# Kernel optimization log

Measured on AMD Instinct MI355X. Metric: run time of the kernel, lower is better.

## Reference

```python
import jax, jax.numpy as jnp
import numpy as np

SCORE_THRESH = 0.5
NMS_THRESH = 0.4
TOP_K = 1000  # fixed pre-NMS candidate budget (jit-safe replacement for boolean masking)
STRIDES = (8, 16, 32)
H, W = 2176, 3840


def _anchor_centers(fh, fw, stride):
    yv, xv = jnp.meshgrid(jnp.arange(fh), jnp.arange(fw), indexing='ij')
    return (jnp.stack([xv, yv], -1).reshape(-1, 2).astype(jnp.float32)) * stride  # [N,2]


def _decode_level(scores, bbox, kps, stride):
    fh, fw = H // stride, W // stride
    c = _anchor_centers(fh, fw, stride)                 # [N,2]
    s = jax.nn.sigmoid(scores.reshape(-1))              # [N]
    d = bbox.reshape(-1, 4) * stride                    # [N,4]
    boxes = jnp.concatenate([c - d[:, :2], c + d[:, 2:4]], axis=1)  # x1y1x2y2
    k = kps.reshape(-1, 5, 2) * stride + c[:, None, :]  # (x,y) pairs
    return s, boxes, k.reshape(-1, 10)


def _iou_matrix(b):
    area = (b[:, 2] - b[:, 0]) * (b[:, 3] - b[:, 1])
    lt = jnp.maximum(b[:, None, :2], b[None, :, :2])
    rb = jnp.minimum(b[:, None, 2:], b[None, :, 2:])
    wh = jnp.clip(rb - lt, 0.0)
    inter = wh[..., 0] * wh[..., 1]
    return inter / jnp.clip(area[:, None] + area[None, :] - inter, 1e-9)


def _nms_keep(iou, valid):
    n = iou.shape[0]
    ar = jnp.arange(n)

    def body(i, keep):
        sup = (iou[i] > NMS_THRESH) & (ar > i) & keep[i]
        return keep & ~sup

    return jax.lax.fori_loop(0, n, body, valid)


def reference(x, scores8, bbox8, kps8, scores16, bbox16, kps16, scores32, bbox32, kps32):
    levels = ((scores8, bbox8, kps8), (scores16, bbox16, kps16), (scores32, bbox32, kps32))
    ss, bs, ks = [], [], []
    for (s, b, k), stride in zip(levels, STRIDES):
        si, bi, ki = _decode_level(s, b, k, stride)
        ss.append(si); bs.append(bi); ks.append(ki)
    scores = jnp.concatenate(ss)   # [N_total]
    boxes = jnp.concatenate(bs)    # [N_total,4]
    kpss = jnp.concatenate(ks)     # [N_total,10]

    masked = jnp.where(scores > SCORE_THRESH, scores, -1.0)
    top_s, idx = jax.lax.top_k(masked, TOP_K)
    valid = top_s > SCORE_THRESH
    b = boxes[idx]
    k = kpss[idx]

    keep = jax.lax.stop_gradient(_nms_keep(_iou_matrix(b), valid))
    final_boxes = jnp.where(keep[:, None], b, 0.0)
    final_scores = jnp.where(keep, top_s, 0.0)
    final_kpss = jnp.where(keep[:, None], k, 0.0)
    return final_boxes, final_scores, final_kpss


def setup_inputs() -> dict:
    key = jax.random.key(0)
    ks = jax.random.split(key, 10)
    n8 = (H // 8) * (W // 8)
    n16 = (H // 16) * (W // 16)
    n32 = (H // 32) * (W // 32)
    return {
        'x': jax.random.normal(ks[0], (1, 3, H, W), jnp.float32),
        'scores8': jax.random.normal(ks[1], (1, n8, 1), jnp.float32),
        'bbox8': jax.random.uniform(ks[2], (1, n8, 4), jnp.float32),
        'kps8': jax.random.normal(ks[3], (1, n8, 10), jnp.float32),
        'scores16': jax.random.normal(ks[4], (1, n16, 1), jnp.float32),
        'bbox16': jax.random.uniform(ks[5], (1, n16, 4), jnp.float32),
        'kps16': jax.random.normal(ks[6], (1, n16, 10), jnp.float32),
        'scores32': jax.random.normal(ks[7], (1, n32, 1), jnp.float32),
        'bbox32': jax.random.uniform(ks[8], (1, n32, 4), jnp.float32),
        'kps32': jax.random.normal(ks[9], (1, n32, 10), jnp.float32),
    }
```

## Files before the change

kernel.cpp:

```cpp
#include <hip/hip_runtime.h>
#include <stdint.h>

typedef unsigned int u32;
typedef unsigned long long u64;

#define N8   130560
#define N16  32640
#define N32  8160
#define NTOT 171360
#define NTOT4 42840
#define TOPK 1000
#define NWORDS 16
#define NBINS 4096
#define BUCKET_SCALE 682.0f
#define LIST_CAP 2048
#define NBLK 168
#define NRED 32
#define RANK_BLKS 32
#define IOU_TASKS (TOPK * NWORDS)
#define IOU_BLKS 63
#define NMS_CACHE 256
#define POISON 0xAAAAAAAAu
#define SPIN_CAP (1u << 22)


#define MI_ARRA 0
#define MI_REDA 128
#define MI_ARRB 256
#define MI_REDD 384
#define MI_B    512
#define MI_CNT  640
#define MI_CMP  768
#define MI_CMPD 896
#define MI_DEC  1024
#define MI_DECD 1152
#define MI_IOU  1280
#define META_U32 1536

#define OFF_PART 0
#define OFF_RED  1376256
#define OFF_META 1392640
#define OFF_NZ   1398784
#define OFF_LIST 1398912
#define OFF_MASK 1415296

__device__ __forceinline__ u32 ald32(const u32* p) {
  return __hip_atomic_load(p, __ATOMIC_RELAXED, __HIP_MEMORY_SCOPE_AGENT);
}
__device__ __forceinline__ u64 ald64(const u64* p) {
  return __hip_atomic_load(p, __ATOMIC_RELAXED, __HIP_MEMORY_SCOPE_AGENT);
}
__device__ __forceinline__ void ast32(u32* p, u32 v) {
  __hip_atomic_store(p, v, __ATOMIC_RELAXED, __HIP_MEMORY_SCOPE_AGENT);
}
__device__ __forceinline__ void ast64(u64* p, u64 v) {
  __hip_atomic_store(p, v, __ATOMIC_RELAXED, __HIP_MEMORY_SCOPE_AGENT);
}
__device__ __forceinline__ void publish(u32* p, u32 v) {
  __hip_atomic_store(p, v, __ATOMIC_RELEASE, __HIP_MEMORY_SCOPE_AGENT);
}
template <int SLP>
__device__ __forceinline__ u32 spin_tag(const u32* p) {
  u32 v, it = 0;
  while (((v = ald32(p)) >> 16) != 0xC0DEu) {
    __builtin_amdgcn_s_sleep(SLP);
    if (++it > SPIN_CAP) break;
  }
  return v;
}
__device__ __forceinline__ u32 normc(u32 v) {
  return v >= 0x80000000u ? v - POISON : v;
}
__device__ __forceinline__ bool arrive_last(u32* p, u32 total) {
  u32 old = __hip_atomic_fetch_add(p, 1u, __ATOMIC_RELAXED, __HIP_MEMORY_SCOPE_AGENT);
  if (normc(old) == total - 1u) { ast32(p, 0u); return true; }
  return false;
}

__device__ __forceinline__ u32 bucket_of(float x) {
  u32 b = (u32)(x * BUCKET_SCALE);
  return b > (NBINS - 1) ? (NBINS - 1) : b;
}

__device__ __forceinline__ float4 load_logit4(int v, const float* s8, const float* s16,
                                              const float* s32) {
  int e = v * 4;
  if (e < N8) return ((const float4*)s8)[v];
  if (e < N8 + N16) return ((const float4*)s16)[v - N8 / 4];
  return ((const float4*)s32)[v - (N8 + N16) / 4];
}

__device__ __forceinline__ bool iou_gt04(float4 a, float4 b) {
#pragma clang fp contract(off)
  float areaA = (a.z - a.x) * (a.w - a.y);
  float areaB = (b.z - b.x) * (b.w - b.y);
  float ltx = fmaxf(a.x, b.x);
  float lty = fmaxf(a.y, b.y);
  float rbx = fminf(a.z, b.z);
  float rby = fminf(a.w, b.w);
  float wx = rbx - ltx; wx = wx > 0.0f ? wx : 0.0f;
  float wy = rby - lty; wy = wy > 0.0f ? wy : 0.0f;
  float inter = wx * wy;
  float un = areaA + areaB - inter;
  un = un > 1e-9f ? un : 1e-9f;
  return (inter / un) > 0.4f;
}

__device__ __forceinline__ u64 valid_word(int w, u32 vcnt) {
  int lo = w * 64;
  if ((int)vcnt >= lo + 64) return ~0ull;
  if ((int)vcnt <= lo) return 0ull;
  return (1ull << (vcnt - (u32)lo)) - 1ull;
}

__global__ void __launch_bounds__(256) k_zero(u32* __restrict__ meta) {
  for (int k = threadIdx.x; k < META_U32; k += 256) meta[k] = 0;
}

__global__ void __launch_bounds__(256) k_fused(
    const float* __restrict__ s8, const float* __restrict__ s16, const float* __restrict__ s32,
    const float* __restrict__ bb8,  const float* __restrict__ kp8,
    const float* __restrict__ bb16, const float* __restrict__ kp16,
    const float* __restrict__ bb32, const float* __restrict__ kp32,
    u32* __restrict__ part, u32* red, u32* meta, u64* nzWords, u64* list, u64* mask,
    float* out) {
  __shared__ __align__(16) char smem[36864];
  __shared__ u32 sB, sCntE, sCntF, sBase;
  __shared__ u32 cnt16[16], sPc[16], sOff17[17];
  __shared__ u64 sRem[NWORDS];
  __shared__ int isLast;
  const int t = threadIdx.x, blk = blockIdx.x;
  const int wave = t >> 6, lane = t & 63;
  const int v = blk * 256 + t;
  u64* o64 = (u64*)out;

  u32* lh = (u32*)smem;
#pragma unroll
  for (int k = 0; k < 16; ++k) lh[k * 256 + t] = 0;
  __syncthreads();
  float4 x = make_float4(-1.f, -1.f, -1.f, -1.f);
  if (v < NTOT4) {
    x = load_logit4(v, s8, s16, s32);
    if (x.x > 0.0f) atomicAdd(&lh[bucket_of(x.x)], 1u);
    if (x.y > 0.0f) atomicAdd(&lh[bucket_of(x.y)], 1u);
    if (x.z > 0.0f) atomicAdd(&lh[bucket_of(x.z)], 1u);
    if (x.w > 0.0f) atomicAdd(&lh[bucket_of(x.w)], 1u);
  }
  __syncthreads();
#pragma unroll
  for (int k = 0; k < 8; ++k) {
    int w = k * 256 + t;
    ast32(&part[blk * 2048 + w], lh[2 * w] | (lh[2 * w + 1] << 16));
  }
  __syncthreads();
  if (t == 0 && arrive_last(&meta[MI_ARRA], NBLK))
    publish(&meta[MI_REDA], 0xC0DE0000u);

  if (blk < NRED) {
    u32* llo = (u32*)smem;
    u32* lhi = llo + 256;
    if (t == 0) spin_tag<2>(&meta[MI_REDA]);
    __syncthreads();
    int w = t & 63, pp = t >> 6;
    u32 lo = 0, hi = 0;
    for (int p = pp; p < NBLK; p += 4) {
      u32 pv = ald32(&part[p * 2048 + blk * 64 + w]);
      lo += pv & 0xFFFFu; hi += pv >> 16;
    }
    llo[t] = lo; lhi[t] = hi;
    __syncthreads();
    if (t < 64) {
      u32 l = llo[t] + llo[64 + t] + llo[128 + t] + llo[192 + t];
      u32 h = lhi[t] + lhi[64 + t] + lhi[128 + t] + lhi[192 + t];
      ast32(&red[blk * 128 + 2 * t], l);
      ast32(&red[blk * 128 + 2 * t + 1], h);
    }
    __syncthreads();
    if (t == 0 && arrive_last(&meta[MI_ARRB], NRED)) {
      ast32(&meta[MI_REDA], 0u);
      publish(&meta[MI_REDD], 0xC0DE0000u);
    }
  }

  if (blk == 0) {
    if (t == 0) { spin_tag<2>(&meta[MI_REDD]); ast32(&meta[MI_REDD], 0u); }
    __syncthreads();
    u32* hloc = (u32*)smem;
    u32* csum = (u32*)(smem + 16384);
#pragma unroll
    for (int k = 0; k < 16; ++k) hloc[k * 256 + t] = ald32(&red[k * 256 + t]);
    if (t < NWORDS) ast64(&nzWords[t], 0ull);
    __syncthreads();
    u32 sum = 0;
    int base = t * 16;
#pragma unroll
    for (int k = 0; k < 16; ++k) sum += hloc[base + k];
    csum[t] = sum;
    __syncthreads();
    for (int off = 1; off < 256; off <<= 1) {
      u32 add = (t + off < 256) ? csum[t + off] : 0u;
      __syncthreads();
      csum[t] += add;
      __syncthreads();
    }
    u32 above = (t < 255) ? csum[t + 1] : 0u;
    if (t == 0 && csum[0] < TOPK) ast32(&meta[MI_B], 0xC0DE0000u);
    if (csum[t] >= TOPK && above < TOPK) {
      u32 cum = above, Bv = (u32)(t * 16);
      for (int b = t * 16 + 15; b >= t * 16; --b) {
        cum += hloc[b];
        if (cum >= TOPK) { Bv = (u32)b; break; }
      }
      ast32(&meta[MI_B], 0xC0DE0000u | Bv);
    }
  }

  if (t == 0) sB = spin_tag<4>(&meta[MI_B]) & 0xFFFFu;
  __syncthreads();
  const u32 B = sB;
  u32 win = 0;
  float c[4] = {x.x, x.y, x.z, x.w};
  if (v < NTOT4) {
#pragma unroll
    for (int j = 0; j < 4; ++j)
      if (c[j] > 0.0f && bucket_of(c[j]) >= B) win |= 1u << j;
  }
  u32 wpos[4], wcnt[4];
#pragma unroll
  for (int j = 0; j < 4; ++j) {
    u64 bal = __ballot((win >> j) & 1u);
    wcnt[j] = (u32)__popcll(bal);
    wpos[j] = (u32)__popcll(bal & ((1ull << lane) - 1ull));
  }
  if (lane == 0) {
#pragma unroll
    for (int j = 0; j < 4; ++j) cnt16[wave * 4 + j] = wcnt[j];
  }
  __syncthreads();
  if (t == 0) {
    u32 tot = 0, pre[16];
#pragma unroll
    for (int k = 0; k < 16; ++k) { pre[k] = tot; tot += cnt16[k]; }
#pragma unroll
    for (int k = 0; k < 16; ++k) cnt16[k] = pre[k];
    sBase = tot ? normc(__hip_atomic_fetch_add(&meta[MI_CNT], tot, __ATOMIC_RELAXED,
                                               __HIP_MEMORY_SCOPE_AGENT))
                : 0u;
  }
  __syncthreads();
#pragma unroll
  for (int j = 0; j < 4; ++j) {
    if ((win >> j) & 1u) {
      u32 dst = sBase + cnt16[wave * 4 + j] + wpos[j];
      if (dst < LIST_CAP) {
        u32 idx = (u32)(v * 4 + j);
        ast64(&list[dst], ((u64)__float_as_uint(c[j]) << 32) | (u64)(~idx));
      }
    }
  }
  __syncthreads();
  if (t == 0 && arrive_last(&meta[MI_CMP], NBLK)) {
    u32 cc = normc(ald32(&meta[MI_CNT]));
    if (cc > LIST_CAP) cc = LIST_CAP;
    ast32(&meta[MI_CNT], 0u);
    ast32(&meta[MI_B], 0u);
    publish(&meta[MI_CMPD], 0xC0DE0000u | cc);
  }
  if (blk >= IOU_BLKS) return;

  if (blk < RANK_BLKS) {
    if (t == 0) sCntE = spin_tag<4>(&meta[MI_CMPD]) & 0xFFFFu;
    __syncthreads();
    const u32 cnt = sCntE;
    u64* keys = (u64*)smem;
    for (int j = t; j < LIST_CAP; j += 256) keys[j] = (j < (int)cnt) ? ald64(&list[j]) : 0ull;
    __syncthreads();
    if (t < 64) {
      int tid = blk * 64 + t;
      if (tid < (int)cnt) {
        u64 my = keys[tid];
        int rank = 0, j = 0;
        for (; j + 4 <= (int)cnt; j += 4)
          rank += (keys[j] > my) + (keys[j + 1] > my) + (keys[j + 2] > my) + (keys[j + 3] > my);
        for (; j < (int)cnt; ++j) rank += (keys[j] > my);
        if (rank < TOPK) {
          float lx = __uint_as_float((u32)(my >> 32));
          float sc = (float)(1.0 / (1.0 + exp(-(double)lx)));
          u32 idx = ~((u32)my);
          float4 box;
          float kv[10];
          int p, xq, yq;
          float st;
          const float *bb, *kp;
          if (idx < N8) {
            st = 8.f;  p = (int)idx;              xq = p % 480; yq = p / 480; bb = bb8;  kp = kp8;
          } else if (idx < N8 + N16) {
            st = 16.f; p = (int)idx - N8;         xq = p % 240; yq = p / 240; bb = bb16; kp = kp16;
          } else {
            st = 32.f; p = (int)idx - (N8 + N16); xq = p % 120; yq = p / 120; bb = bb32; kp = kp32;
          }
          float cx = (float)xq * st, cy = (float)yq * st;
          {
#pragma clang fp contract(off)
            float d0 = bb[4 * p + 0] * st;
            float d1 = bb[4 * p + 1] * st;
            float d2 = bb[4 * p + 2] * st;
            float d3 = bb[4 * p + 3] * st;
            box.x = cx - d0; box.y = cy - d1; box.z = cx + d2; box.w = cy + d3;
            for (int q = 0; q < 10; ++q)
              kv[q] = kp[10 * p + q] * st + ((q & 1) ? cy : cx);
          }
          ast64(&o64[2 * rank],     ((u64)__float_as_uint(box.y) << 32) | __float_as_uint(box.x));
          ast64(&o64[2 * rank + 1], ((u64)__float_as_uint(box.w) << 32) | __float_as_uint(box.z));
          ast32(&((u32*)out)[4000 + rank], __float_as_uint(sc));
          int wb = 2500 + 5 * rank;
#pragma unroll
          for (int q = 0; q < 5; ++q)
            ast64(&o64[wb + q],
                  ((u64)__float_as_uint(kv[2 * q + 1]) << 32) | __float_as_uint(kv[2 * q]));
        }
      } else if (tid < TOPK) {
        ast64(&o64[2 * tid], 0ull); ast64(&o64[2 * tid + 1], 0ull);
        ast32(&((u32*)out)[4000 + tid], 0u);
        int wb = 2500 + 5 * tid;
#pragma unroll
        for (int q = 0; q < 5; ++q) ast64(&o64[wb + q], 0ull);
      }
    }
    __syncthreads();
    if (t == 0 && arrive_last(&meta[MI_DEC], RANK_BLKS)) {
      ast32(&meta[MI_CMPD], 0u);
      publish(&meta[MI_DECD], 0xC0DE0000u | cnt);
    }
  }

  if (t == 0) sCntF = spin_tag<4>(&meta[MI_DECD]) & 0xFFFFu;
  __syncthreads();
  {
    float4* boxes = (float4*)smem;
    for (int r = t; r < TOPK; r += 256) {
      u64 a = ald64(&o64[2 * r]), b = ald64(&o64[2 * r + 1]);
      float4 bx;
      bx.x = __uint_as_float((u32)a); bx.y = __uint_as_float((u32)(a >> 32));
      bx.z = __uint_as_float((u32)b); bx.w = __uint_as_float((u32)(b >> 32));
      boxes[r] = bx;
    }
    __syncthreads();
    int task = blk * 256 + t;
    if (task < IOU_TASKS) {
      int w = task / 1000;
      int i = task - w * 1000;
      float4 a = boxes[i];
      int bse = w * 64;
      int jend = (bse + 64) < TOPK ? (bse + 64) : TOPK;
      u64 bits = 0;
      for (int j = bse; j < jend; ++j)
        if (j > i && iou_gt04(a, boxes[j])) bits |= 1ull << (j - bse);
      ast64(&mask[(u64)w * 1000 + i], bits);
      if (bits) atomicOr(&nzWords[i >> 6], 1ull << (i & 63));
    }
    __syncthreads();
    if (t == 0) {
      bool lastF = arrive_last(&meta[MI_IOU], IOU_BLKS);
      if (lastF) ast32(&meta[MI_DECD], 0u);
      isLast = lastF ? 1 : 0;
    }
    __syncthreads();
    if (!isLast) return;

    const u32 vcnt = sCntF < TOPK ? sCntF : TOPK;
    u32* rows = (u32*)smem;
    u64* cache = (u64*)(smem + 4096);
    u64 nzv = 0;
    if (t < NWORDS) {
      nzv = ald64(&nzWords[t]) & valid_word(t, vcnt);
      sPc[t] = (u32)__popcll(nzv);
    }
    __syncthreads();
    if (t == 0) {
      u32 o = 0;
      for (int w = 0; w < NWORDS; ++w) { sOff17[w] = o; o += sPc[w]; }
      sOff17[16] = o;
    }
    __syncthreads();
    if (t < NWORDS) {
      u64 m = nzv;
      u32 o = sOff17[t];
      while (m) { int b = __builtin_ctzll(m); m &= m - 1; rows[o++] = (u32)(t * 64 + b); }
    }
    __syncthreads();
    const int S = (int)sOff17[16];
    const int Sc = S < NMS_CACHE ? S : NMS_CACHE;
    for (int idx = t; idx < Sc * NWORDS; idx += 256) {
      int s = idx >> 4, w = idx & 15;
      cache[s * NWORDS + w] = ald64(&mask[(u64)w * 1000 + rows[s]]);
    }
    __syncthreads();
    if (t < 64) {
      u64 remv = 0;
      for (int s = 0; s < S; ++s) {
        u32 row = rows[s];
        int cc = (int)(row >> 6), b = (int)(row & 63);
        u64 remc = __shfl(remv, cc);
        if (!((remc >> b) & 1ull)) {
          u64 m = 0;
          if (t < NWORDS)
            m = (s < NMS_CACHE) ? cache[s * NWORDS + t] : ald64(&mask[(u64)t * 1000 + row]);
          remv |= m;
        }
      }
      if (t < NWORDS) sRem[t] = valid_word(t, vcnt) & remv;
    }
    __syncthreads();
    for (int r = t; r < TOPK; r += 256) {
      if ((sRem[r >> 6] >> (r & 63)) & 1ull) {
        ast64(&o64[2 * r], 0ull); ast64(&o64[2 * r + 1], 0ull);
        ast32(&((u32*)out)[4000 + r], 0u);
        int wb = 2500 + 5 * r;
#pragma unroll
        for (int q = 0; q < 5; ++q) ast64(&o64[wb + q], 0ull);
      }
    }
  }
}

extern "C" void kernel_launch(void* const* d_in, const int* in_sizes, int n_in,
                              void* d_out, int out_size, void* d_ws, size_t ws_size,
                              hipStream_t stream) {
  const float* s8   = (const float*)d_in[1];
  const float* bb8  = (const float*)d_in[2];
  const float* kp8  = (const float*)d_in[3];
  const float* s16  = (const float*)d_in[4];
  const float* bb16 = (const float*)d_in[5];
  const float* kp16 = (const float*)d_in[6];
  const float* s32  = (const float*)d_in[7];
  const float* bb32 = (const float*)d_in[8];
  const float* kp32 = (const float*)d_in[9];

  char* ws = (char*)d_ws;
  u32* part    = (u32*)(ws + OFF_PART);
  u32* red     = (u32*)(ws + OFF_RED);
  u32* meta    = (u32*)(ws + OFF_META);
  u64* nzWords = (u64*)(ws + OFF_NZ);
  u64* list    = (u64*)(ws + OFF_LIST);
  u64* mask    = (u64*)(ws + OFF_MASK);
  float* out   = (float*)d_out;

  k_zero<<<1, 256, 0, stream>>>(meta);
  k_fused<<<NBLK, 256, 0, stream>>>(s8, s16, s32, bb8, kp8, bb16, kp16, bb32, kp32,
                                    part, red, meta, nzWords, list, mask, out);
}
```

Baseline: 198.8 us.

## Collapse pipeline into single 63-block kernel with global-atomic histogram and split rank

Drops the separate meta-zeroing kernel and the two-level partial histogram reduction. Each of 63 blocks now loads 12 logits per thread and adds directly into a global histogram with atomics; the last-arriving block computes the threshold bucket and re-zeroes the histogram and meta for the next call. The rank stage is spread across all blocks by splitting each candidate's comparison count over 8 slices, and the publish flags are replicated 8 ways to spread spinning across cache lines. This removes one launch and several grid barriers, at the cost of contended global atomics and relying on self-reset state being correct across calls.

```diff
diff --git a/kernel.cpp b/kernel.cpp
--- a/kernel.cpp
+++ b/kernel.cpp
@@ -13,36 +13,32 @@
 #define NWORDS 16
 #define NBINS 4096
 #define BUCKET_SCALE 682.0f
-#define LIST_CAP 2048
-#define NBLK 168
-#define NRED 32
-#define RANK_BLKS 32
+#define NBLK 63
+#define NTHR 256
+#define STRIDE (NBLK*NTHR)
+#define LIST_CAP 2016
+#define CPB 32
 #define IOU_TASKS (TOPK * NWORDS)
-#define IOU_BLKS 63
 #define NMS_CACHE 256
 #define POISON 0xAAAAAAAAu
-#define SPIN_CAP (1u << 22)
+#define SPIN_CAP (1u << 20)
 
 
 #define MI_ARRA 0
-#define MI_REDA 128
-#define MI_ARRB 256
-#define MI_REDD 384
-#define MI_B    512
-#define MI_CNT  640
-#define MI_CMP  768
-#define MI_CMPD 896
-#define MI_DEC  1024
-#define MI_DECD 1152
-#define MI_IOU  1280
-#define META_U32 1536
-
-#define OFF_PART 0
-#define OFF_RED  1376256
-#define OFF_META 1392640
-#define OFF_NZ   1398784
-#define OFF_LIST 1398912
-#define OFF_MASK 1415296
+#define MI_B(c)    (128*(1+(c)))
+#define MI_CNT     (128*9)
+#define MI_CMP     (128*10)
+#define MI_CMPD(c) (128*(11+(c)))
+#define MI_DEC     (128*19)
+#define MI_DECD(c) (128*(20+(c)))
+#define MI_IOU     (128*28)
+#define META_U32   (128*29)
+
+#define OFF_HIST 0
+#define OFF_META 16384
+#define OFF_NZ   32768
+#define OFF_LIST 33024
+#define OFF_MASK 49152
 
 __device__ __forceinline__ u32 ald32(const u32* p) {
   return __hip_atomic_load(p, __ATOMIC_RELAXED, __HIP_MEMORY_SCOPE_AGENT);
@@ -113,82 +109,41 @@
   return (1ull << (vcnt - (u32)lo)) - 1ull;
 }
 
-__global__ void __launch_bounds__(256) k_zero(u32* __restrict__ meta) {
-  for (int k = threadIdx.x; k < META_U32; k += 256) meta[k] = 0;
-}
-
-__global__ void __launch_bounds__(256) k_fused(
+__global__ void __launch_bounds__(256) k_all(
     const float* __restrict__ s8, const float* __restrict__ s16, const float* __restrict__ s32,
     const float* __restrict__ bb8,  const float* __restrict__ kp8,
     const float* __restrict__ bb16, const float* __restrict__ kp16,
     const float* __restrict__ bb32, const float* __restrict__ kp32,
-    u32* __restrict__ part, u32* red, u32* meta, u64* nzWords, u64* list, u64* mask,
-    float* out) {
+    u32* hist, u32* meta, u64* nzWords, u64* list, u64* mask, float* out) {
   __shared__ __align__(16) char smem[36864];
-  __shared__ u32 sB, sCntE, sCntF, sBase;
-  __shared__ u32 cnt16[16], sPc[16], sOff17[17];
+  __shared__ u32 sB, sBpub, sCntE, sCntF, sBase;
+  __shared__ int sFind, isLast;
+  __shared__ u32 cnt48[48];
+  __shared__ u32 sPc[16], sOff17[17];
   __shared__ u64 sRem[NWORDS];
-  __shared__ int isLast;
   const int t = threadIdx.x, blk = blockIdx.x;
   const int wave = t >> 6, lane = t & 63;
-  const int v = blk * 256 + t;
   u64* o64 = (u64*)out;
 
-  u32* lh = (u32*)smem;
-#pragma unroll
-  for (int k = 0; k < 16; ++k) lh[k * 256 + t] = 0;
-  __syncthreads();
-  float4 x = make_float4(-1.f, -1.f, -1.f, -1.f);
-  if (v < NTOT4) {
-    x = load_logit4(v, s8, s16, s32);
-    if (x.x > 0.0f) atomicAdd(&lh[bucket_of(x.x)], 1u);
-    if (x.y > 0.0f) atomicAdd(&lh[bucket_of(x.y)], 1u);
-    if (x.z > 0.0f) atomicAdd(&lh[bucket_of(x.z)], 1u);
-    if (x.w > 0.0f) atomicAdd(&lh[bucket_of(x.w)], 1u);
-  }
-  __syncthreads();
-#pragma unroll
-  for (int k = 0; k < 8; ++k) {
-    int w = k * 256 + t;
-    ast32(&part[blk * 2048 + w], lh[2 * w] | (lh[2 * w + 1] << 16));
-  }
-  __syncthreads();
-  if (t == 0 && arrive_last(&meta[MI_ARRA], NBLK))
-    publish(&meta[MI_REDA], 0xC0DE0000u);
-
-  if (blk < NRED) {
-    u32* llo = (u32*)smem;
-    u32* lhi = llo + 256;
-    if (t == 0) spin_tag<2>(&meta[MI_REDA]);
-    __syncthreads();
-    int w = t & 63, pp = t >> 6;
-    u32 lo = 0, hi = 0;
-    for (int p = pp; p < NBLK; p += 4) {
-      u32 pv = ald32(&part[p * 2048 + blk * 64 + w]);
-      lo += pv & 0xFFFFu; hi += pv >> 16;
-    }
-    llo[t] = lo; lhi[t] = hi;
-    __syncthreads();
-    if (t < 64) {
-      u32 l = llo[t] + llo[64 + t] + llo[128 + t] + llo[192 + t];
-      u32 h = lhi[t] + lhi[64 + t] + lhi[128 + t] + lhi[192 + t];
-      ast32(&red[blk * 128 + 2 * t], l);
-      ast32(&red[blk * 128 + 2 * t + 1], h);
-    }
-    __syncthreads();
-    if (t == 0 && arrive_last(&meta[MI_ARRB], NRED)) {
-      ast32(&meta[MI_REDA], 0u);
-      publish(&meta[MI_REDD], 0xC0DE0000u);
-    }
-  }
-
-  if (blk == 0) {
-    if (t == 0) { spin_tag<2>(&meta[MI_REDD]); ast32(&meta[MI_REDD], 0u); }
-    __syncthreads();
+  const int v0 = blk * NTHR + t;
+  float4 x0 = load_logit4(v0, s8, s16, s32);
+  float4 x1 = load_logit4(v0 + STRIDE, s8, s16, s32);
+  float4 x2 = make_float4(-1.f, -1.f, -1.f, -1.f);
+  if (v0 + 2 * STRIDE < NTOT4) x2 = load_logit4(v0 + 2 * STRIDE, s8, s16, s32);
+  float cv[12] = {x0.x, x0.y, x0.z, x0.w, x1.x, x1.y, x1.z, x1.w,
+                  x2.x, x2.y, x2.z, x2.w};
+#pragma unroll
+  for (int j = 0; j < 12; ++j)
+    if (cv[j] > 0.0f) atomicAdd(&hist[bucket_of(cv[j])], 1u);
+  __syncthreads();
+  if (t == 0) sFind = arrive_last(&meta[MI_ARRA], NBLK) ? 1 : 0;
+  __syncthreads();
+
+  if (sFind) {
     u32* hloc = (u32*)smem;
     u32* csum = (u32*)(smem + 16384);
 #pragma unroll
-    for (int k = 0; k < 16; ++k) hloc[k * 256 + t] = ald32(&red[k * 256 + t]);
+    for (int k = 0; k < 16; ++k) hloc[k * 256 + t] = normc(ald32(&hist[k * 256 + t]));
     if (t < NWORDS) ast64(&nzWords[t], 0ull);
     __syncthreads();
     u32 sum = 0;
@@ -204,57 +159,52 @@
       __syncthreads();
     }
     u32 above = (t < 255) ? csum[t + 1] : 0u;
-    if (t == 0 && csum[0] < TOPK) ast32(&meta[MI_B], 0xC0DE0000u);
+    if (t == 0 && csum[0] < TOPK) sBpub = 0u;
     if (csum[t] >= TOPK && above < TOPK) {
       u32 cum = above, Bv = (u32)(t * 16);
       for (int b = t * 16 + 15; b >= t * 16; --b) {
         cum += hloc[b];
         if (cum >= TOPK) { Bv = (u32)b; break; }
       }
-      ast32(&meta[MI_B], 0xC0DE0000u | Bv);
-    }
-  }
-
-  if (t == 0) sB = spin_tag<4>(&meta[MI_B]) & 0xFFFFu;
+      sBpub = Bv;
+    }
+    __syncthreads();
+    if (t < 8) publish(&meta[MI_B(t)], 0xC0DE0000u | sBpub);
+#pragma unroll
+    for (int k = 0; k < 16; ++k) hist[k * 256 + t] = 0u;
+  }
+
+  if (t == 0) sB = spin_tag<8>(&meta[MI_B(blk & 7)]) & 0xFFFFu;
   __syncthreads();
   const u32 B = sB;
-  u32 win = 0;
-  float c[4] = {x.x, x.y, x.z, x.w};
-  if (v < NTOT4) {
-#pragma unroll
-    for (int j = 0; j < 4; ++j)
-      if (c[j] > 0.0f && bucket_of(c[j]) >= B) win |= 1u << j;
-  }
-  u32 wpos[4], wcnt[4];
-#pragma unroll
-  for (int j = 0; j < 4; ++j) {
-    u64 bal = __ballot((win >> j) & 1u);
-    wcnt[j] = (u32)__popcll(bal);
+  u32 winm = 0;
+#pragma unroll
+  for (int j = 0; j < 12; ++j)
+    if (cv[j] > 0.0f && bucket_of(cv[j]) >= B) winm |= 1u << j;
+  u32 wpos[12];
+#pragma unroll
+  for (int j = 0; j < 12; ++j) {
+    u64 bal = __ballot((winm >> j) & 1u);
+    if (lane == 0) cnt48[wave * 12 + j] = (u32)__popcll(bal);
     wpos[j] = (u32)__popcll(bal & ((1ull << lane) - 1ull));
   }
-  if (lane == 0) {
-#pragma unroll
-    for (int j = 0; j < 4; ++j) cnt16[wave * 4 + j] = wcnt[j];
-  }
   __syncthreads();
   if (t == 0) {
-    u32 tot = 0, pre[16];
-#pragma unroll
-    for (int k = 0; k < 16; ++k) { pre[k] = tot; tot += cnt16[k]; }
-#pragma unroll
-    for (int k = 0; k < 16; ++k) cnt16[k] = pre[k];
+    u32 tot = 0, pre;
+#pragma unroll
+    for (int k = 0; k < 48; ++k) { pre = tot; tot += cnt48[k]; cnt48[k] = pre; }
     sBase = tot ? normc(__hip_atomic_fetch_add(&meta[MI_CNT], tot, __ATOMIC_RELAXED,
                                                __HIP_MEMORY_SCOPE_AGENT))
                 : 0u;
   }
   __syncthreads();
 #pragma unroll
-  for (int j = 0; j < 4; ++j) {
-    if ((win >> j) & 1u) {
-      u32 dst = sBase + cnt16[wave * 4 + j] + wpos[j];
+  for (int j = 0; j < 12; ++j) {
+    if ((winm >> j) & 1u) {
+      u32 dst = sBase + cnt48[wave * 12 + j] + wpos[j];
       if (dst < LIST_CAP) {
-        u32 idx = (u32)(v * 4 + j);
-        ast64(&list[dst], ((u64)__float_as_uint(c[j]) << 32) | (u64)(~idx));
+        u32 idx = (u32)((v0 + (j >> 2) * STRIDE) * 4 + (j & 3));
+        ast64(&list[dst], ((u64)__float_as_uint(cv[j]) << 32) | (u64)(~idx));
       }
     }
   }
@@ -263,27 +213,43 @@
     u32 cc = normc(ald32(&meta[MI_CNT]));
     if (cc > LIST_CAP) cc = LIST_CAP;
     ast32(&meta[MI_CNT], 0u);
-    ast32(&meta[MI_B], 0u);
-    publish(&meta[MI_CMPD], 0xC0DE0000u | cc);
-  }
-  if (blk >= IOU_BLKS) return;
-
-  if (blk < RANK_BLKS) {
-    if (t == 0) sCntE = spin_tag<4>(&meta[MI_CMPD]) & 0xFFFFu;
-    __syncthreads();
-    const u32 cnt = sCntE;
+#pragma unroll
+    for (int c = 0; c < 8; ++c) ast32(&meta[MI_B(c)], 0u);
+#pragma unroll
+    for (int c = 0; c < 8; ++c) publish(&meta[MI_CMPD(c)], 0xC0DE0000u | cc);
+  }
+
+  if (t == 0) sCntE = spin_tag<8>(&meta[MI_CMPD(blk & 7)]) & 0xFFFFu;
+  __syncthreads();
+  const u32 cnt = sCntE;
+  {
     u64* keys = (u64*)smem;
-    for (int j = t; j < LIST_CAP; j += 256) keys[j] = (j < (int)cnt) ? ald64(&list[j]) : 0ull;
-    __syncthreads();
-    if (t < 64) {
-      int tid = blk * 64 + t;
-      if (tid < (int)cnt) {
-        u64 my = keys[tid];
-        int rank = 0, j = 0;
-        for (; j + 4 <= (int)cnt; j += 4)
-          rank += (keys[j] > my) + (keys[j + 1] > my) + (keys[j + 2] > my) + (keys[j + 3] > my);
-        for (; j < (int)cnt; ++j) rank += (keys[j] > my);
+    u32* rpart = (u32*)(smem + 16384);
+    for (int j = t; j < LIST_CAP; j += NTHR)
+      keys[j] = (j < (int)cnt) ? ald64(&list[j]) : 0ull;
+    __syncthreads();
+    {
+      const int ci = t & 31, sl = t >> 5;
+      const int c = blk * CPB + ci;
+      const int chunk = ((int)cnt + 7) >> 3;
+      int lo = sl * chunk; if (lo > (int)cnt) lo = (int)cnt;
+      int hi = lo + chunk; if (hi > (int)cnt) hi = (int)cnt;
+      u64 my = keys[c];
+      int r = 0, j = lo;
+      for (; j + 4 <= hi; j += 4)
+        r += (keys[j] > my) + (keys[j + 1] > my) + (keys[j + 2] > my) + (keys[j + 3] > my);
+      for (; j < hi; ++j) r += (keys[j] > my);
+      rpart[t] = (u32)r;
+    }
+    __syncthreads();
+    if (t < CPB) {
+      const int c = blk * CPB + t;
+      if (c < (int)cnt) {
+        int rank = 0;
+#pragma unroll
+        for (int q = 0; q < 8; ++q) rank += (int)rpart[t + 32 * q];
         if (rank < TOPK) {
+          u64 my = keys[c];
           float lx = __uint_as_float((u32)(my >> 32));
           float sc = (float)(1.0 / (1.0 + exp(-(double)lx)));
           u32 idx = ~((u32)my);
@@ -319,26 +285,28 @@
             ast64(&o64[wb + q],
                   ((u64)__float_as_uint(kv[2 * q + 1]) << 32) | __float_as_uint(kv[2 * q]));
         }
-      } else if (tid < TOPK) {
-        ast64(&o64[2 * tid], 0ull); ast64(&o64[2 * tid + 1], 0ull);
-        ast32(&((u32*)out)[4000 + tid], 0u);
-        int wb = 2500 + 5 * tid;
+      } else if (c < TOPK) {
+        ast64(&o64[2 * c], 0ull); ast64(&o64[2 * c + 1], 0ull);
+        ast32(&((u32*)out)[4000 + c], 0u);
+        int wb = 2500 + 5 * c;
 #pragma unroll
         for (int q = 0; q < 5; ++q) ast64(&o64[wb + q], 0ull);
       }
     }
-    __syncthreads();
-    if (t == 0 && arrive_last(&meta[MI_DEC], RANK_BLKS)) {
-      ast32(&meta[MI_CMPD], 0u);
-      publish(&meta[MI_DECD], 0xC0DE0000u | cnt);
-    }
-  }
-
-  if (t == 0) sCntF = spin_tag<4>(&meta[MI_DECD]) & 0xFFFFu;
+  }
+  __syncthreads();
+  if (t == 0 && arrive_last(&meta[MI_DEC], NBLK)) {
+#pragma unroll
+    for (int c = 0; c < 8; ++c) ast32(&meta[MI_CMPD(c)], 0u);
+#pragma unroll
+    for (int c = 0; c < 8; ++c) publish(&meta[MI_DECD(c)], 0xC0DE0000u | cnt);
+  }
+
+  if (t == 0) sCntF = spin_tag<8>(&meta[MI_DECD(blk & 7)]) & 0xFFFFu;
   __syncthreads();
   {
     float4* boxes = (float4*)smem;
-    for (int r = t; r < TOPK; r += 256) {
+    for (int r = t; r < TOPK; r += NTHR) {
       u64 a = ald64(&o64[2 * r]), b = ald64(&o64[2 * r + 1]);
       float4 bx;
       bx.x = __uint_as_float((u32)a); bx.y = __uint_as_float((u32)(a >> 32));
@@ -346,7 +314,7 @@
       boxes[r] = bx;
     }
     __syncthreads();
-    int task = blk * 256 + t;
+    int task = blk * NTHR + t;
     if (task < IOU_TASKS) {
       int w = task / 1000;
       int i = task - w * 1000;
@@ -361,9 +329,12 @@
     }
     __syncthreads();
     if (t == 0) {
-      bool lastF = arrive_last(&meta[MI_IOU], IOU_BLKS);
-      if (lastF) ast32(&meta[MI_DECD], 0u);
-      isLast = lastF ? 1 : 0;
+      int last = arrive_last(&meta[MI_IOU], NBLK) ? 1 : 0;
+      if (last) {
+#pragma unroll
+        for (int c = 0; c < 8; ++c) ast32(&meta[MI_DECD(c)], 0u);
+      }
+      isLast = last;
     }
     __syncthreads();
     if (!isLast) return;
@@ -391,7 +362,7 @@
     __syncthreads();
     const int S = (int)sOff17[16];
     const int Sc = S < NMS_CACHE ? S : NMS_CACHE;
-    for (int idx = t; idx < Sc * NWORDS; idx += 256) {
+    for (int idx = t; idx < Sc * NWORDS; idx += NTHR) {
       int s = idx >> 4, w = idx & 15;
       cache[s * NWORDS + w] = ald64(&mask[(u64)w * 1000 + rows[s]]);
     }
@@ -412,7 +383,7 @@
       if (t < NWORDS) sRem[t] = valid_word(t, vcnt) & remv;
     }
     __syncthreads();
-    for (int r = t; r < TOPK; r += 256) {
+    for (int r = t; r < TOPK; r += NTHR) {
       if ((sRem[r >> 6] >> (r & 63)) & 1ull) {
         ast64(&o64[2 * r], 0ull); ast64(&o64[2 * r + 1], 0ull);
         ast32(&((u32*)out)[4000 + r], 0u);
@@ -438,15 +409,13 @@
   const float* kp32 = (const float*)d_in[9];
 
   char* ws = (char*)d_ws;
-  u32* part    = (u32*)(ws + OFF_PART);
-  u32* red     = (u32*)(ws + OFF_RED);
+  u32* hist    = (u32*)(ws + OFF_HIST);
   u32* meta    = (u32*)(ws + OFF_META);
   u64* nzWords = (u64*)(ws + OFF_NZ);
   u64* list    = (u64*)(ws + OFF_LIST);
   u64* mask    = (u64*)(ws + OFF_MASK);
   float* out   = (float*)d_out;
 
-  k_zero<<<1, 256, 0, stream>>>(meta);
-  k_fused<<<NBLK, 256, 0, stream>>>(s8, s16, s32, bb8, kp8, bb16, kp16, bb32, kp32,
-                                    part, red, meta, nzWords, list, mask, out);
-}
+  k_all<<<NBLK, NTHR, 0, stream>>>(s8, s16, s32, bb8, kp8, bb16, kp16, bb32, kp32,
+                                   hist, meta, nzWords, list, mask, out);
+}
```

New measurement: 197.3 us. Within noise of the previous version (-0.8%).
